# Performance work log

Measured on AMD Instinct MI355X. Metric: run time of the kernel, lower is better.

Reference implementation:

```python
import jax, jax.numpy as jnp
import numpy as np

NUM_HEADS = 16
D_MODEL = 1024
D_K = D_MODEL // NUM_HEADS
EPS = 1e-6


def setup_inputs() -> dict:
    key = jax.random.key(0)
    ks = jax.random.split(key, 12)
    B, S, D = 8, 1024, D_MODEL
    scale = 0.02
    return {
        "query": jax.random.normal(ks[0], (B, S, D), dtype=jnp.float32),
        "key": jax.random.normal(ks[1], (B, S, D), dtype=jnp.float32),
        "value": jax.random.normal(ks[2], (B, S, D), dtype=jnp.float32),
        "policy": jax.random.uniform(ks[3], (B, S, 1), dtype=jnp.float32),
        "wq_w": jax.random.normal(ks[4], (D, D), dtype=jnp.float32) * scale,
        "wq_b": jnp.zeros((D,), dtype=jnp.float32),
        "wk_w": jax.random.normal(ks[5], (D, D), dtype=jnp.float32) * scale,
        "wk_b": jnp.zeros((D,), dtype=jnp.float32),
        "wv_w": jax.random.normal(ks[6], (D, D), dtype=jnp.float32) * scale,
        "wv_b": jnp.zeros((D,), dtype=jnp.float32),
        "dense_w": jax.random.normal(ks[7], (D, D), dtype=jnp.float32) * scale,
        "dense_b": jnp.zeros((D,), dtype=jnp.float32),
    }


def _split_heads(x):
    B, S, D = x.shape
    return x.reshape(B, S, NUM_HEADS, D_K).transpose(0, 2, 1, 3)  # [B,H,S,dk]


def reference(query, key, value, policy, wq_w, wq_b, wk_w, wk_b, wv_w, wv_b, dense_w, dense_b):
    B, S, D = query.shape
    # torch Linear: y = x @ W.T + b
    q = _split_heads(query @ wq_w.T + wq_b)
    k = _split_heads(key @ wk_w.T + wk_b)
    v = _split_heads(value @ wv_w.T + wv_b)

    scores = jnp.einsum("bhqd,bhkd->bhqk", q, k) / jnp.sqrt(jnp.float32(D_K))
    # policy branch: exp * policy normalization (no softmax max-subtraction, faithful)
    attn_policy = policy.reshape(B, 1, 1, S)
    sc = jnp.exp(scores) * attn_policy
    p_attn = (sc + EPS / S) / (jnp.sum(sc, axis=-1, keepdims=True) + EPS)

    x = jnp.einsum("bhqk,bhkd->bhqd", p_attn, v)
    x = x.transpose(0, 2, 1, 3).reshape(B, S, D)
    out = x @ dense_w.T + dense_b  # dropout = identity (eval mode)
    return out
```

## Files before the change

### kernel.cpp

```cpp
#include <hip/hip_runtime.h>


#define Sdim 1024
#define Ddim 1024

typedef unsigned short u16;
typedef float f32x4 __attribute__((ext_vector_type(4)));
typedef float f32x16 __attribute__((ext_vector_type(16)));
typedef __bf16 bf16x8 __attribute__((ext_vector_type(8)));
typedef u16 u16x8 __attribute__((ext_vector_type(8)));
typedef unsigned u32x2 __attribute__((ext_vector_type(2)));
typedef __attribute__((address_space(3))) void lds_void;
typedef __attribute__((address_space(1))) void gbl_void;

__device__ __forceinline__ u16 f2bf(float f) {
    unsigned u = __float_as_uint(f);
    u += 0x7fffu + ((u >> 16) & 1u);
    return (u16)(u >> 16);
}
__device__ __forceinline__ void gld16(const void* g, void* l) {
    __builtin_amdgcn_global_load_lds((const gbl_void*)g, (lds_void*)l, 16, 0, 0);
}
__device__ __forceinline__ float fexp2(float x) {
#if __has_builtin(__builtin_amdgcn_exp2f)
    return __builtin_amdgcn_exp2f(x);
#else
    return __expf(x * 0.6931471805599453f);
#endif
}
__device__ __forceinline__ unsigned cvtpk(float lo, float hi) {
    unsigned r;
    asm("v_cvt_pk_bf16_f32 %0, %1, %2" : "=v"(r) : "v"(lo), "v"(hi));
    return r;
}
#define MFMA16(a, b, c) __builtin_amdgcn_mfma_f32_16x16x32_bf16((a), (b), (c), 0, 0, 0)
#define MFMA32(a, b, c) __builtin_amdgcn_mfma_f32_32x32x16_bf16((a), (b), (c), 0, 0, 0)
#define SCHEDB() __builtin_amdgcn_sched_barrier(0)

#define QSCALE 0.18033688011112042f

__global__ __launch_bounds__(256) void cvt_all(const float* __restrict__ s0,
                                               const float* __restrict__ s1,
                                               const float* __restrict__ s2,
                                               const float* __restrict__ s3,
                                               const float* __restrict__ s4,
                                               const float* __restrict__ s5,
                                               const float* __restrict__ s6,
                                               u16* __restrict__ d0, u16* __restrict__ d1,
                                               u16* __restrict__ d2, u16* __restrict__ d3,
                                               u16* __restrict__ d4, u16* __restrict__ d5,
                                               u16* __restrict__ d6) {
    const int z = blockIdx.y;
    if (z >= 3 && blockIdx.x >= 512) return;
    const float* s = z == 0 ? s0 : z == 1 ? s1 : z == 2 ? s2 : z == 3 ? s3
                   : z == 4 ? s4 : z == 5 ? s5 : s6;
    u16* d = z == 0 ? d0 : z == 1 ? d1 : z == 2 ? d2 : z == 3 ? d3
           : z == 4 ? d4 : z == 5 ? d5 : d6;
    const float sc = (z == 3) ? QSCALE : 1.0f;
    const int i = (blockIdx.x * 256 + threadIdx.x) * 8;
    const float4 a = *(const float4*)(s + i);
    const float4 b = *(const float4*)(s + i + 4);
    u16x8 o;
    o[0] = f2bf(a.x * sc); o[1] = f2bf(a.y * sc); o[2] = f2bf(a.z * sc); o[3] = f2bf(a.w * sc);
    o[4] = f2bf(b.x * sc); o[5] = f2bf(b.y * sc); o[6] = f2bf(b.z * sc); o[7] = f2bf(b.w * sc);
    *(u16x8*)(d + i) = o;
}

template <bool OUT_BF16>
__device__ __forceinline__ void gemm2p_body(const u16* __restrict__ A,
                                            const u16* __restrict__ W,
                                            const float* __restrict__ bias, float bscale,
                                            void* __restrict__ Cout,
                                            char* __restrict__ smem,
                                            int m0, int n0) {
    const int tid  = threadIdx.x;
    const int w    = tid >> 6;
    const int lane = tid & 63;
    const int l15  = lane & 15;
    const int quad = lane >> 4;
    const int wr   = w >> 1;
    const int wc   = w & 1;

    const int lrow = lane >> 3;
    const int scol = (((lane & 7) ^ lrow) << 3);
    const u16* pa = A + (size_t)(m0 + w * 32 + lrow) * Ddim + scol;
    const u16* pb = W + (size_t)(n0 + w * 16 + lrow) * Ddim + scol;
    char* sAw = smem + w * 4096;
    char* sBw = smem + 65536 + w * 2048;

#define STG(t, b)                                                             \
    do {                                                                      \
        const int k0 = (t) * 64;                                              \
        gld16(pa + k0,             sAw + (b) * 32768);                        \
        gld16(pa + k0 + 8 * 1024,  sAw + (b) * 32768 + 1024);                 \
        gld16(pa + k0 + 16 * 1024, sAw + (b) * 32768 + 2048);                 \
        gld16(pa + k0 + 24 * 1024, sAw + (b) * 32768 + 3072);                 \
        gld16(pb + k0,             sBw + (b) * 16384);                        \
        gld16(pb + k0 + 8 * 1024,  sBw + (b) * 16384 + 1024);                 \
    } while (0)

    const char* Ab = smem + (size_t)(wr * 64 + l15) * 128;
    const char* Bb = smem + 65536 + (size_t)(wc * 64 + l15) * 128;
    const int cx = ((quad ^ (l15 & 7)) << 4);

    f32x4 acc[4][4] = {};

    STG(0, 0);
    __syncthreads();

    for (int t = 0; t < 16; ++t) {
        const int boA = (t & 1) * 32768;
        const int boB = (t & 1) * 16384;
        if (t < 15) STG(t + 1, (t & 1) ^ 1);
        SCHEDB();
#pragma unroll
        for (int ks = 0; ks < 2; ++ks) {
            const int cxs = cx ^ (ks << 6);
            bf16x8 af[4], bfr[4];
#pragma unroll
            for (int i = 0; i < 4; ++i)
                af[i] = *(const bf16x8*)(Ab + boA + i * 2048 + cxs);
#pragma unroll
            for (int j = 0; j < 4; ++j)
                bfr[j] = *(const bf16x8*)(Bb + boB + j * 2048 + cxs);
#pragma unroll
            for (int i = 0; i < 4; ++i)
#pragma unroll
                for (int j = 0; j < 4; ++j)
                    acc[i][j] = MFMA16(af[i], bfr[j], acc[i][j]);
        }
        __syncthreads();
    }
#undef STG

    float bv[4];
#pragma unroll
    for (int j = 0; j < 4; ++j)
        bv[j] = bias[n0 + wc * 64 + j * 16 + l15] * bscale;
#pragma unroll
    for (int i = 0; i < 4; ++i)
#pragma unroll
        for (int j = 0; j < 4; ++j)
#pragma unroll
            for (int r = 0; r < 4; ++r) {
                const int row = m0 + wr * 64 + i * 16 + quad * 4 + r;
                const int col = n0 + wc * 64 + j * 16 + l15;
                const float v = acc[i][j][r] + bv[j];
                if (OUT_BF16)
                    ((u16*)Cout)[(size_t)row * Ddim + col] = f2bf(v);
                else
                    ((float*)Cout)[(size_t)row * Ddim + col] = v;
            }
}

__global__ __launch_bounds__(512, 2) void gemm2p_qkv(
        const u16* __restrict__ A0, const u16* __restrict__ A1, const u16* __restrict__ A2,
        const u16* __restrict__ W0, const u16* __restrict__ W1, const u16* __restrict__ W2,
        const float* __restrict__ b0, const float* __restrict__ b1, const float* __restrict__ b2,
        u16* __restrict__ C0, u16* __restrict__ C1, u16* __restrict__ C2) {
    __shared__ __align__(16) char smem[98304];
    const int d = blockIdx.x;
    const int s = (d & 7) * 96 + (d >> 3);
    const int z = s >> 8;
    const int rr = s & 255;
    const int tm = rr >> 3, tn = rr & 7;
    const u16* A = z == 0 ? A0 : z == 1 ? A1 : A2;
    const u16* W = z == 0 ? W0 : z == 1 ? W1 : W2;
    const float* bias = z == 0 ? b0 : z == 1 ? b1 : b2;
    u16* C = z == 0 ? C0 : z == 1 ? C1 : C2;
    const float bsc = (z == 0) ? QSCALE : 1.0f;
    gemm2p_body<true>(A, W, bias, bsc, (void*)C, smem, tm * 256, tn * 128);
}

__global__ __launch_bounds__(512, 2) void gemm2p_dense(const u16* __restrict__ A,
                                                       const u16* __restrict__ W,
                                                       const float* __restrict__ bias,
                                                       float* __restrict__ C) {
    __shared__ __align__(16) char smem[98304];
    const int d = blockIdx.x;
    const int s = (d & 7) * 32 + (d >> 3);
    const int tm = s >> 3, tn = s & 7;
    gemm2p_body<false>(A, W, bias, 1.0f, (void*)C, smem, tm * 256, tn * 128);
}

__global__ __launch_bounds__(256) void transp_v(const u16* __restrict__ Vp,
                                                u16* __restrict__ Vt) {
    __shared__ __align__(16) u16 Ts[64][72];
    const int bh = blockIdx.x, s0 = blockIdx.y * 64;
    const int b = bh >> 4, h = bh & 15;
    const int tid = threadIdx.x;
#pragma unroll
    for (int p = 0; p < 2; ++p) {
        const int e = p * 2048 + tid * 8;
        const int r = e >> 6, c = e & 63;
        *(u16x8*)&Ts[r][c] =
            *(const u16x8*)(Vp + ((size_t)(b * Sdim + s0 + r)) * Ddim + h * 64 + c);
    }
    __syncthreads();
    const int d = tid >> 2, sp = tid & 3;
#pragma unroll
    for (int g = 0; g < 2; ++g) {
        u16x8 o;
#pragma unroll
        for (int j = 0; j < 8; ++j) o[j] = Ts[sp * 16 + g * 8 + j][d];
        *(u16x8*)(Vt + ((size_t)(bh * 64 + d)) * Sdim + s0 + sp * 16 + g * 8) = o;
    }
}

__global__ __launch_bounds__(256, 2) void attn_mfma(const u16* __restrict__ Qp,
                                                    const u16* __restrict__ Kp,
                                                    const u16* __restrict__ Vt,
                                                    const float* __restrict__ pol,
                                                    u16* __restrict__ Xb) {
    __shared__ __align__(16) u16 lds[37632];
    u16* Qs = lds;
    u16* Ks = lds + 18432;
    u16* Vs = lds + 27648;
    float* pols = (float*)(lds + 36864);
    float* denb = pols + 128;

    const int tid  = threadIdx.x;
    const int w    = tid >> 6;
    const int lane = tid & 63;
    const int l31  = lane & 31;
    const unsigned hsel = lane >> 5;
    const int bh = blockIdx.x;
    const int q0 = blockIdx.y * 256;
    const size_t bS = (size_t)(bh >> 4) * Sdim;
    const int col0 = (bh & 15) * 64;
    const int sr = tid >> 2;
    const int sc4 = tid & 3;

    const u16* Kg = Kp + (bS + sr) * Ddim + col0 + sc4 * 8;
    const u16* Vg = Vt + ((size_t)(bh * 64 + sr)) * Sdim + sc4 * 8;
    const float* pg = pol + bS + tid;

#pragma unroll
    for (int rg = 0; rg < 4; ++rg) {
        const int r = rg * 64 + sr;
#pragma unroll
        for (int g = 0; g < 2; ++g) {
            const int ch = sc4 + g * 4;
            *(u16x8*)(Qs + r * 72 + ch * 8) =
                *(const u16x8*)(Qp + (bS + q0 + r) * Ddim + col0 + ch * 8);
        }
    }
#pragma unroll
    for (int g = 0; g < 2; ++g) {
        *(u16x8*)(Ks + sr * 72 + (sc4 + g * 4) * 8) = *(const u16x8*)(Kg + g * 32);
        *(u16x8*)(Vs + sr * 72 + (sc4 + g * 4) * 8) = *(const u16x8*)(Vg + g * 32);
    }
    if (tid < 64) pols[tid] = pg[0];
    __syncthreads();

    bf16x8 Qf[2][4];
#pragma unroll
    for (int qt = 0; qt < 2; ++qt)
#pragma unroll
        for (int dkt = 0; dkt < 4; ++dkt)
            Qf[qt][dkt] = *(const bf16x8*)(Qs + (w * 64 + qt * 32 + l31) * 72 +
                                           dkt * 16 + hsel * 8);

    f32x16 X[2][2] = {};
    float den[2] = {0.f, 0.f};

    for (int kt = 0; kt < 16; ++kt) {
        const int cur = kt & 1;
        const bool pf = (kt < 15);
        u16x8 kr0 = {}, kr1 = {}, vr0 = {}, vr1 = {};
        float polr = 0.f;
        if (pf) {
            const int ko = (kt + 1) * 64;
            kr0 = *(const u16x8*)(Kg + (size_t)ko * Ddim);
            kr1 = *(const u16x8*)(Kg + (size_t)ko * Ddim + 32);
            vr0 = *(const u16x8*)(Vg + ko);
            vr1 = *(const u16x8*)(Vg + ko + 32);
            if (tid < 64) polr = pg[ko];
        }
        SCHEDB();

        const u16* Ksc = Ks + cur * 4608;
        const u16* Vsc = Vs + cur * 4608;
        const float* polc = pols + cur * 64;
#pragma unroll
        for (int t32 = 0; t32 < 2; ++t32) {
            float polv[16];
#pragma unroll
            for (int e = 0; e < 16; ++e)
                polv[e] = polc[t32 * 32 + (e & 3) + 8 * (e >> 2) + 4 * hsel];
            bf16x8 Kf[4];
#pragma unroll
            for (int dkt = 0; dkt < 4; ++dkt)
                Kf[dkt] = *(const bf16x8*)(Ksc + (t32 * 32 + l31) * 72 +
                                           dkt * 16 + hsel * 8);
#pragma unroll
            for (int qt = 0; qt < 2; ++qt) {
                f32x16 S = {};
#pragma unroll
                for (int dkt = 0; dkt < 4; ++dkt)
                    S = MFMA32(Kf[dkt], Qf[qt][dkt], S);
                float p[16];
#pragma unroll
                for (int e = 0; e < 16; ++e) {
                    p[e] = fexp2(S[e]) * polv[e];
                    den[qt] += p[e];
                }
                unsigned pk_[8];
#pragma unroll
                for (int g = 0; g < 4; ++g) {
                    pk_[2 * g]     = cvtpk(p[4 * g + 0], p[4 * g + 1]);
                    pk_[2 * g + 1] = cvtpk(p[4 * g + 2], p[4 * g + 3]);
                }
#pragma unroll
                for (int tau = 0; tau < 2; ++tau) {
                    const u32x2 sA = __builtin_amdgcn_permlane32_swap(
                        pk_[4 * tau + 0], pk_[4 * tau + 2], false, false);
                    const u32x2 sB = __builtin_amdgcn_permlane32_swap(
                        pk_[4 * tau + 1], pk_[4 * tau + 3], false, false);
                    union { unsigned u[4]; bf16x8 v; } Af;
                    Af.u[0] = sA[0]; Af.u[1] = sB[0];
                    Af.u[2] = sA[1]; Af.u[3] = sB[1];
#pragma unroll
                    for (int ndt = 0; ndt < 2; ++ndt) {
                        const bf16x8 Vf =
                            *(const bf16x8*)(Vsc + (ndt * 32 + l31) * 72 +
                                             t32 * 32 + tau * 16 + hsel * 8);
                        X[qt][ndt] = MFMA32(Af.v, Vf, X[qt][ndt]);
                    }
                }
            }
        }
        if (pf) {
            const int nxt = cur ^ 1;
            *(u16x8*)(Ks + nxt * 4608 + sr * 72 + sc4 * 8) = kr0;
            *(u16x8*)(Ks + nxt * 4608 + sr * 72 + (sc4 + 4) * 8) = kr1;
            *(u16x8*)(Vs + nxt * 4608 + sr * 72 + sc4 * 8) = vr0;
            *(u16x8*)(Vs + nxt * 4608 + sr * 72 + (sc4 + 4) * 8) = vr1;
            if (tid < 64) pols[nxt * 64 + tid] = polr;
        }
        __syncthreads();
    }

#pragma unroll
    for (int qt = 0; qt < 2; ++qt) {
        den[qt] += __shfl_xor(den[qt], 32);
        denb[w * 64 + qt * 32 + l31] = 1.0f / (den[qt] + 1e-6f);
    }
    u16* Xout = Qs;
#pragma unroll
    for (int qt = 0; qt < 2; ++qt) {
        float invv[16];
#pragma unroll
        for (int e = 0; e < 16; ++e)
            invv[e] = denb[w * 64 + qt * 32 + (e & 3) + 8 * (e >> 2) + 4 * hsel];
#pragma unroll
        for (int ndt = 0; ndt < 2; ++ndt)
#pragma unroll
            for (int e = 0; e < 16; ++e) {
                const int rho = (e & 3) + 8 * (e >> 2) + 4 * hsel;
                Xout[(w * 64 + qt * 32 + rho) * 72 + ndt * 32 + l31] =
                    f2bf(X[qt][ndt][e] * invv[e]);
            }
    }
    __syncthreads();
#pragma unroll
    for (int rg = 0; rg < 4; ++rg) {
        const int r = rg * 64 + sr;
#pragma unroll
        for (int g = 0; g < 2; ++g) {
            const int ch = sc4 + g * 4;
            *(u16x8*)(Xb + (bS + q0 + r) * Ddim + col0 + ch * 8) =
                *(const u16x8*)(Xout + r * 72 + ch * 8);
        }
    }
}

extern "C" void kernel_launch(void* const* d_in, const int* in_sizes, int n_in,
                              void* d_out, int out_size, void* d_ws, size_t ws_size,
                              hipStream_t stream) {
    const float* query   = (const float*)d_in[0];
    const float* key     = (const float*)d_in[1];
    const float* value   = (const float*)d_in[2];
    const float* policy  = (const float*)d_in[3];
    const float* wq_w    = (const float*)d_in[4];
    const float* wq_b    = (const float*)d_in[5];
    const float* wk_w    = (const float*)d_in[6];
    const float* wk_b    = (const float*)d_in[7];
    const float* wv_w    = (const float*)d_in[8];
    const float* wv_b    = (const float*)d_in[9];
    const float* dense_w = (const float*)d_in[10];
    const float* dense_b = (const float*)d_in[11];

    const size_t MM = 1u << 20;
    const size_t A8 = 8 * MM;
    u16* qa  = (u16*)d_ws;
    u16* ka  = qa + A8;
    u16* va  = ka + A8;
    u16* wqb = va + A8;
    u16* wkb = wqb + MM;
    u16* wvb = wkb + MM;
    u16* wdb = wvb + MM;
    u16* Qp  = wdb + MM;
    u16* Kp  = Qp + A8;
    u16* Vp  = Kp + A8;
    u16* Vtg = ka;
    u16* Xb  = qa;

    cvt_all<<<dim3(4096, 7), 256, 0, stream>>>(query, key, value, wq_w, wk_w, wv_w, dense_w,
                                               qa, ka, va, wqb, wkb, wvb, wdb);

    gemm2p_qkv<<<dim3(768), 512, 0, stream>>>(qa, ka, va, wqb, wkb, wvb,
                                              wq_b, wk_b, wv_b, Qp, Kp, Vp);
    transp_v<<<dim3(128, 16), 256, 0, stream>>>(Vp, Vtg);

    attn_mfma<<<dim3(128, 4), 256, 0, stream>>>(Qp, Kp, Vtg, policy, Xb);

    gemm2p_dense<<<dim3(256), 512, 0, stream>>>(Xb, wdb, dense_b, (float*)d_out);
}
```

Baseline: 295.0 us.

## Load GEMM B operand directly from global into registers, shrink LDS

```diff
diff --git a/kernel.cpp b/kernel.cpp
--- a/kernel.cpp
+++ b/kernel.cpp
@@ -67,12 +67,12 @@
 }
 
 template <bool OUT_BF16>
-__device__ __forceinline__ void gemm2p_body(const u16* __restrict__ A,
-                                            const u16* __restrict__ W,
-                                            const float* __restrict__ bias, float bscale,
-                                            void* __restrict__ Cout,
-                                            char* __restrict__ smem,
-                                            int m0, int n0) {
+__device__ __forceinline__ void gemm_bd_body(const u16* __restrict__ A,
+                                             const u16* __restrict__ W,
+                                             const float* __restrict__ bias, float bscale,
+                                             void* __restrict__ Cout,
+                                             char* __restrict__ smem,
+                                             int m0, int n0) {
     const int tid  = threadIdx.x;
     const int w    = tid >> 6;
     const int lane = tid & 63;
@@ -84,51 +84,51 @@
     const int lrow = lane >> 3;
     const int scol = (((lane & 7) ^ lrow) << 3);
     const u16* pa = A + (size_t)(m0 + w * 32 + lrow) * Ddim + scol;
-    const u16* pb = W + (size_t)(n0 + w * 16 + lrow) * Ddim + scol;
     char* sAw = smem + w * 4096;
-    char* sBw = smem + 65536 + w * 2048;
-
-#define STG(t, b)                                                             \
+
+#define STG(b)                                                                \
     do {                                                                      \
-        const int k0 = (t) * 64;                                              \
-        gld16(pa + k0,             sAw + (b) * 32768);                        \
-        gld16(pa + k0 + 8 * 1024,  sAw + (b) * 32768 + 1024);                 \
-        gld16(pa + k0 + 16 * 1024, sAw + (b) * 32768 + 2048);                 \
-        gld16(pa + k0 + 24 * 1024, sAw + (b) * 32768 + 3072);                 \
-        gld16(pb + k0,             sBw + (b) * 16384);                        \
-        gld16(pb + k0 + 8 * 1024,  sBw + (b) * 16384 + 1024);                 \
+        gld16(pa,             sAw + (b) * 32768);                             \
+        gld16(pa + 8 * 1024,  sAw + (b) * 32768 + 1024);                      \
+        gld16(pa + 16 * 1024, sAw + (b) * 32768 + 2048);                      \
+        gld16(pa + 24 * 1024, sAw + (b) * 32768 + 3072);                      \
+        pa += 64;                                                             \
     } while (0)
 
     const char* Ab = smem + (size_t)(wr * 64 + l15) * 128;
-    const char* Bb = smem + 65536 + (size_t)(wc * 64 + l15) * 128;
     const int cx = ((quad ^ (l15 & 7)) << 4);
 
+    const u16* Wt = W + (size_t)(n0 + wc * 64 + l15) * Ddim + quad * 8;
+
     f32x4 acc[4][4] = {};
 
-    STG(0, 0);
+    STG(0);
     __syncthreads();
 
     for (int t = 0; t < 16; ++t) {
         const int boA = (t & 1) * 32768;
-        const int boB = (t & 1) * 16384;
-        if (t < 15) STG(t + 1, (t & 1) ^ 1);
+        bf16x8 bf[2][4];
+#pragma unroll
+        for (int ks = 0; ks < 2; ++ks)
+#pragma unroll
+            for (int j = 0; j < 4; ++j)
+                bf[ks][j] = *(const bf16x8*)(Wt + (size_t)(j * 16) * Ddim + ks * 32);
+        if (t < 15) STG((t & 1) ^ 1);
         SCHEDB();
 #pragma unroll
         for (int ks = 0; ks < 2; ++ks) {
             const int cxs = cx ^ (ks << 6);
-            bf16x8 af[4], bfr[4];
+            bf16x8 af[4];
 #pragma unroll
             for (int i = 0; i < 4; ++i)
                 af[i] = *(const bf16x8*)(Ab + boA + i * 2048 + cxs);
 #pragma unroll
-            for (int j = 0; j < 4; ++j)
-                bfr[j] = *(const bf16x8*)(Bb + boB + j * 2048 + cxs);
-#pragma unroll
             for (int i = 0; i < 4; ++i)
 #pragma unroll
                 for (int j = 0; j < 4; ++j)
-                    acc[i][j] = MFMA16(af[i], bfr[j], acc[i][j]);
-        }
+                    acc[i][j] = MFMA16(af[i], bf[ks][j], acc[i][j]);
+        }
+        Wt += 64;
         __syncthreads();
     }
 #undef STG
@@ -153,12 +153,12 @@
             }
 }
 
-__global__ __launch_bounds__(512, 2) void gemm2p_qkv(
+__global__ __launch_bounds__(512, 4) void gemm2p_qkv(
         const u16* __restrict__ A0, const u16* __restrict__ A1, const u16* __restrict__ A2,
         const u16* __restrict__ W0, const u16* __restrict__ W1, const u16* __restrict__ W2,
         const float* __restrict__ b0, const float* __restrict__ b1, const float* __restrict__ b2,
         u16* __restrict__ C0, u16* __restrict__ C1, u16* __restrict__ C2) {
-    __shared__ __align__(16) char smem[98304];
+    __shared__ __align__(16) char smem[65536];
     const int d = blockIdx.x;
     const int s = (d & 7) * 96 + (d >> 3);
     const int z = s >> 8;
@@ -169,18 +169,18 @@
     const float* bias = z == 0 ? b0 : z == 1 ? b1 : b2;
     u16* C = z == 0 ? C0 : z == 1 ? C1 : C2;
     const float bsc = (z == 0) ? QSCALE : 1.0f;
-    gemm2p_body<true>(A, W, bias, bsc, (void*)C, smem, tm * 256, tn * 128);
-}
-
-__global__ __launch_bounds__(512, 2) void gemm2p_dense(const u16* __restrict__ A,
+    gemm_bd_body<true>(A, W, bias, bsc, (void*)C, smem, tm * 256, tn * 128);
+}
+
+__global__ __launch_bounds__(512, 4) void gemm2p_dense(const u16* __restrict__ A,
                                                        const u16* __restrict__ W,
                                                        const float* __restrict__ bias,
                                                        float* __restrict__ C) {
-    __shared__ __align__(16) char smem[98304];
+    __shared__ __align__(16) char smem[65536];
     const int d = blockIdx.x;
     const int s = (d & 7) * 32 + (d >> 3);
     const int tm = s >> 3, tn = s & 7;
-    gemm2p_body<false>(A, W, bias, 1.0f, (void*)C, smem, tm * 256, tn * 128);
+    gemm_bd_body<false>(A, W, bias, 1.0f, (void*)C, smem, tm * 256, tn * 128);
 }
 
 __global__ __launch_bounds__(256) void transp_v(const u16* __restrict__ Vp,
```

Result: slower. 375.6 us (+27.3%).
